# Kernel optimization log

Hardware: AMD Instinct MI355X
Metric: run time of the kernel (lower is better)

Reference implementation:

```python
import jax, jax.numpy as jnp
import numpy as np

N_NODES = 50000
N_EDGES = 800000
D_IN = 96
HID = 128


def _glorot(key, shape):
    fan_in, fan_out = shape[0], shape[1]
    lim = np.sqrt(6.0 / (fan_in + fan_out)).astype(np.float32)
    return jax.random.uniform(key, shape, jnp.float32, -lim, lim)


def setup_inputs() -> dict:
    key = jax.random.key(0)
    ks = jax.random.split(key, 12)
    x = jax.random.normal(ks[0], (N_NODES, D_IN), jnp.float32)
    edge_index = jax.random.randint(ks[1], (2, N_EDGES), 0, N_NODES)
    return {
        "x": x,
        "edge_index": edge_index,
        "W_in": _glorot(ks[2], (D_IN, HID)),
        "b_in": jnp.zeros((HID,), jnp.float32),
        "W1": _glorot(ks[3], (HID, HID)),
        "b1": jnp.zeros((HID,), jnp.float32),
        "W2": _glorot(ks[4], (HID, HID)),
        "b2": jnp.zeros((HID,), jnp.float32),
        "Wm1": _glorot(ks[5], (2 * HID, HID)),
        "bm1": jnp.zeros((HID,), jnp.float32),
        "Wm2": _glorot(ks[6], (HID, 1)),
        "bm2": jnp.zeros((1,), jnp.float32),
    }


def _gcn_conv(h, W, b, src, dst, n_nodes):
    # PyG GCNConv with add_self_loops=True, normalize=True:
    # out = D^{-1/2} (A + I) D^{-1/2} (h W) + b, aggregating x_j (source) into dst.
    loop = jnp.arange(n_nodes)
    row = jnp.concatenate([src, loop])  # source / j
    col = jnp.concatenate([dst, loop])  # target / i
    deg = jax.ops.segment_sum(jnp.ones(row.shape, h.dtype), col, num_segments=n_nodes)
    dinv = jnp.where(deg > 0, jax.lax.rsqrt(deg), 0.0)
    norm = dinv[row] * dinv[col]  # [E+N]
    xw = h @ W  # [N, H]
    msg = xw[row] * norm[:, None]  # gather + scale, [E+N, H]
    out = jax.ops.segment_sum(msg, col, num_segments=n_nodes)  # scatter-add
    return out + b


def reference(x, edge_index, W_in, b_in, W1, b1, W2, b2, Wm1, bm1, Wm2, bm2):
    src, dst = edge_index[0], edge_index[1]
    n = x.shape[0]
    h = jax.nn.relu(x @ W_in + b_in)  # dropout is identity at inference
    h = jax.nn.relu(_gcn_conv(h, W1, b1, src, dst, n))
    h = jax.nn.relu(_gcn_conv(h, W2, b2, src, dst, n))
    ef = jnp.concatenate([h[src], h[dst]], axis=1)  # [E, 2H]
    hid = jax.nn.relu(ef @ Wm1 + bm1)
    logits = (hid @ Wm2 + bm2)[:, 0]  # [E]
    return logits
```

## Files before the change

### kernel.cpp

```cpp
#include <hip/hip_runtime.h>

#define N_NODES 50000
#define N_EDGES 800000
#define D_IN 96
#define HID 128
#define NB 391
#define BCAP 3072

typedef __attribute__((ext_vector_type(8))) _Float16 halfx8;
typedef __attribute__((ext_vector_type(2))) _Float16 half2v;
typedef __attribute__((ext_vector_type(16))) float f32x16;

__global__ __launch_bounds__(256) void bucket_hist_kernel(const int* __restrict__ dst,
                                                          int* __restrict__ bhist) {
    __shared__ int lh[NB];
    int t = threadIdx.x;
    for (int i = t; i < NB; i += 256) lh[i] = 0;
    __syncthreads();
    int base = blockIdx.x * 4096;
#pragma unroll
    for (int i = 0; i < 16; i++) {
        int e = base + i * 256 + t;
        if (e < N_EDGES) atomicAdd(&lh[dst[e] >> 7], 1);
    }
    __syncthreads();
    for (int i = t; i < NB; i += 256) atomicAdd(&bhist[i], lh[i]);
}

__global__ __launch_bounds__(512) void scan_buckets_kernel(const int* __restrict__ bhist,
                                                           int* __restrict__ boff,
                                                           int* __restrict__ bcursor) {
    __shared__ int s[512];
    int t = threadIdx.x;
    int v = (t < NB) ? bhist[t] : 0;
    s[t] = v;
    __syncthreads();
    for (int off = 1; off < 512; off <<= 1) {
        int u = (t >= off) ? s[t - off] : 0;
        __syncthreads();
        s[t] += u;
        __syncthreads();
    }
    if (t < NB) {
        int ex = s[t] - v;
        boff[t] = ex;
        bcursor[t] = ex;
    }
    if (t == NB - 1) boff[NB] = s[t];
}

__global__ __launch_bounds__(512) void bin_kernel(const int* __restrict__ src,
                                                  const int* __restrict__ dst,
                                                  int* __restrict__ bcursor,
                                                  unsigned long long* __restrict__ binned) {
    __shared__ int lh[NB];
    __shared__ int gbs[NB];
    int t = threadIdx.x;
    for (int i = t; i < NB; i += 512) lh[i] = 0;
    __syncthreads();
    int base = blockIdx.x * 8192;
    unsigned long long pk[16];
    int bb[16], rk[16];
#pragma unroll
    for (int i = 0; i < 16; i++) {
        int e = base + i * 512 + t;
        bb[i] = -1;
        if (e < N_EDGES) {
            int s = src[e], d = dst[e];
            int b = d >> 7;
            bb[i] = b;
            pk[i] = ((unsigned long long)s << 27) |
                    ((unsigned long long)(d & 127) << 20) | (unsigned long long)e;
            rk[i] = atomicAdd(&lh[b], 1);
        }
    }
    __syncthreads();
    for (int i = t; i < NB; i += 512) gbs[i] = atomicAdd(&bcursor[i], lh[i]);
    __syncthreads();
#pragma unroll
    for (int i = 0; i < 16; i++) {
        if (bb[i] >= 0) binned[gbs[bb[i]] + rk[i]] = pk[i];
    }
}

__global__ __launch_bounds__(256) void bucket_sort_kernel(const unsigned long long* __restrict__ binned,
                                                          const int* __restrict__ boff,
                                                          int2* __restrict__ ce_se,
                                                          int* __restrict__ ce_dst,
                                                          int* __restrict__ csr_ptr,
                                                          float* __restrict__ dinv) {
    __shared__ unsigned long long ed[BCAP];
    __shared__ int2 sorted[BCAP];
    __shared__ int cntA[128], sc[128];
    int b = blockIdx.x;
    int t = threadIdx.x;
    int base = boff[b];
    int k = boff[b + 1] - base;
    if (k > BCAP) k = BCAP;
    if (t < 128) cntA[t] = 0;
    __syncthreads();
    int rk[12], li[12];
    int nmine = 0;
    for (int i = t; i < k; i += 256) {
        unsigned long long p = binned[base + i];
        ed[i] = p;
        int d = (int)((p >> 20) & 127);
        rk[nmine] = atomicAdd(&cntA[d], 1);
        li[nmine] = i;
        nmine++;
    }
    __syncthreads();
    if (t < 128) sc[t] = cntA[t];
    __syncthreads();
    for (int off = 1; off < 128; off <<= 1) {
        int u = 0;
        if (t < 128 && t >= off) u = sc[t - off];
        __syncthreads();
        if (t < 128) sc[t] += u;
        __syncthreads();
    }
    for (int m = 0; m < nmine; m++) {
        unsigned long long p = ed[li[m]];
        int d = (int)((p >> 20) & 127);
        int pos = sc[d] - cntA[d] + rk[m];
        int srcn = (int)(p >> 27);
        int eid = (int)(p & 0xFFFFF);
        sorted[pos] = make_int2(srcn | (d << 16), eid);
    }
    __syncthreads();
    for (int i = t; i < k; i += 256) {
        int2 se = sorted[i];
        ce_se[base + i] = make_int2(se.x & 0xFFFF, se.y);
        ce_dst[base + i] = (b << 7) + (se.x >> 16);
    }
    if (t < 128) {
        int node = (b << 7) + t;
        if (node < N_NODES) {
            csr_ptr[node] = base + sc[t] - cntA[t];
            dinv[node] = 1.0f / sqrtf((float)(cntA[t] + 1));
        }
    }
    if (b == NB - 1 && t == 0) csr_ptr[N_NODES] = boff[NB];
}

__global__ __launch_bounds__(256) void pack_weights_kernel(const float* __restrict__ W_in,
                                                           const float* __restrict__ W1,
                                                           const float* __restrict__ W2,
                                                           const float* __restrict__ Wm1,
                                                           _Float16* __restrict__ packed) {
    int t = blockIdx.x * 256 + threadIdx.x;
    const float* Wsrc;
    int K, u;
    if (t < 12288)      { Wsrc = W_in;            K = 96;  u = t; }
    else if (t < 28672) { Wsrc = W1;              K = 128; u = t - 12288; }
    else if (t < 45056) { Wsrc = W2;              K = 128; u = t - 28672; }
    else if (t < 61440) { Wsrc = Wm1;             K = 128; u = t - 45056; }
    else                { Wsrc = Wm1 + 128 * 128; K = 128; u = t - 61440; }
    if (t >= 77824) return;
    int steps = K >> 4;
    int cb = u / (steps * 512);
    int rem = u - cb * steps * 512;
    int s = rem >> 9;
    int lane = (rem >> 3) & 63;
    int j = rem & 7;
    int k = s * 16 + ((lane >> 5) << 3) + j;
    int n = (cb << 5) + (lane & 31);
    packed[t] = (_Float16)Wsrc[k * 128 + n];
}

__global__ __launch_bounds__(256) void fused_in_kernel(const float* __restrict__ x,
                                                       const _Float16* __restrict__ WpIn,
                                                       const _Float16* __restrict__ Wp1,
                                                       const float* __restrict__ b_in,
                                                       const float* __restrict__ dinv,
                                                       _Float16* __restrict__ y1, int M) {
    __shared__ _Float16 As[64 * 104];
    __shared__ _Float16 Hs[64 * 136];
    int tid = threadIdx.x;
    int M0 = blockIdx.x * 64;
    for (int i = tid; i < 64 * 24; i += 256) {
        int r = i / 24, c = i - r * 24;
        float4 v = make_float4(0.f, 0.f, 0.f, 0.f);
        int row = M0 + r;
        if (row < M) v = *(const float4*)&x[(size_t)row * 96 + c * 4];
        half2v a = {(_Float16)v.x, (_Float16)v.y};
        half2v b = {(_Float16)v.z, (_Float16)v.w};
        *(half2v*)&As[r * 104 + c * 4] = a;
        *(half2v*)&As[r * 104 + c * 4 + 2] = b;
    }
    __syncthreads();

    int wave = tid >> 6, lane = tid & 63;
    int rb = wave & 1;
    int cb0 = (wave >> 1) * 2;
    int colA = cb0 * 32 + (lane & 31);
    int colB = colA + 32;
    {
        const halfx8* bp0 = (const halfx8*)WpIn + (size_t)cb0 * 6 * 64 + lane;
        const halfx8* bp1 = bp0 + (size_t)6 * 64;
        const _Float16* arow = &As[(rb * 32 + (lane & 31)) * 104 + ((lane >> 5) << 3)];
        f32x16 acc0 = {}, acc1 = {};
#pragma unroll
        for (int s = 0; s < 6; s++) {
            halfx8 a = *(const halfx8*)&arow[s * 16];
            acc0 = __builtin_amdgcn_mfma_f32_32x32x16_f16(a, bp0[s * 64], acc0, 0, 0, 0);
            acc1 = __builtin_amdgcn_mfma_f32_32x32x16_f16(a, bp1[s * 64], acc1, 0, 0, 0);
        }
        float bA = b_in[colA], bB = b_in[colB];
#pragma unroll
        for (int r = 0; r < 16; r++) {
            int rl = (r & 3) + 8 * (r >> 2) + 4 * (lane >> 5);
            int lrow = rb * 32 + rl;
            Hs[lrow * 136 + colA] = (_Float16)fmaxf(acc0[r] + bA, 0.f);
            Hs[lrow * 136 + colB] = (_Float16)fmaxf(acc1[r] + bB, 0.f);
        }
    }
    __syncthreads();
    {
        const halfx8* bp0 = (const halfx8*)Wp1 + (size_t)cb0 * 8 * 64 + lane;
        const halfx8* bp1 = bp0 + (size_t)8 * 64;
        const _Float16* arow = &Hs[(rb * 32 + (lane & 31)) * 136 + ((lane >> 5) << 3)];
        f32x16 acc0 = {}, acc1 = {};
#pragma unroll
        for (int s = 0; s < 8; s++) {
            halfx8 a = *(const halfx8*)&arow[s * 16];
            acc0 = __builtin_amdgcn_mfma_f32_32x32x16_f16(a, bp0[s * 64], acc0, 0, 0, 0);
            acc1 = __builtin_amdgcn_mfma_f32_32x32x16_f16(a, bp1[s * 64], acc1, 0, 0, 0);
        }
#pragma unroll
        for (int r = 0; r < 16; r++) {
            int rl = (r & 3) + 8 * (r >> 2) + 4 * (lane >> 5);
            int grow = M0 + rb * 32 + rl;
            if (grow < M) {
                float sc = dinv[grow];
                y1[(size_t)grow * 128 + colA] = (_Float16)(acc0[r] * sc);
                y1[(size_t)grow * 128 + colB] = (_Float16)(acc1[r] * sc);
            }
        }
    }
}

__global__ __launch_bounds__(256) void gemm_f16_kernel(const _Float16* __restrict__ A,
                                                       const _Float16* __restrict__ Wp,
                                                       const float* __restrict__ bias,
                                                       const float* __restrict__ rowscale,
                                                       _Float16* __restrict__ out,
                                                       int M, int K, int steps, int dorelu) {
    __shared__ _Float16 As[64 * 136];
    int tid = threadIdx.x;
    int M0 = blockIdx.x * 64;
    int stride = K + 8;
    int CH = K >> 3;
    int tot = 64 * CH;
    for (int i = tid; i < tot; i += 256) {
        int r = i / CH, c = i - r * CH;
        uint4 v = make_uint4(0, 0, 0, 0);
        int row = M0 + r;
        if (row < M) v = *(const uint4*)&A[(size_t)row * K + c * 8];
        *(uint4*)&As[r * stride + c * 8] = v;
    }
    __syncthreads();

    int wave = tid >> 6, lane = tid & 63;
    int rb = wave & 1;
    int cb0 = (wave >> 1) * 2;
    const halfx8* bp0 = (const halfx8*)Wp + (size_t)cb0 * steps * 64 + lane;
    const halfx8* bp1 = bp0 + (size_t)steps * 64;
    const _Float16* arow = &As[(rb * 32 + (lane & 31)) * stride + ((lane >> 5) << 3)];
    f32x16 acc0 = {}, acc1 = {};
    for (int s = 0; s < steps; s++) {
        halfx8 a = *(const halfx8*)&arow[s * 16];
        acc0 = __builtin_amdgcn_mfma_f32_32x32x16_f16(a, bp0[s * 64], acc0, 0, 0, 0);
        acc1 = __builtin_amdgcn_mfma_f32_32x32x16_f16(a, bp1[s * 64], acc1, 0, 0, 0);
    }

    int colA = cb0 * 32 + (lane & 31);
    int colB = colA + 32;
    float bA = bias ? bias[colA] : 0.f;
    float bB = bias ? bias[colB] : 0.f;
#pragma unroll
    for (int r = 0; r < 16; r++) {
        int rl = (r & 3) + 8 * (r >> 2) + 4 * (lane >> 5);
        int grow = M0 + rb * 32 + rl;
        if (grow < M) {
            float sc = rowscale ? rowscale[grow] : 1.f;
            float v0 = (acc0[r] + bA) * sc;
            float v1 = (acc1[r] + bB) * sc;
            if (dorelu) { v0 = fmaxf(v0, 0.f); v1 = fmaxf(v1, 0.f); }
            out[(size_t)grow * 128 + colA] = (_Float16)v0;
            out[(size_t)grow * 128 + colB] = (_Float16)v1;
        }
    }
}

__global__ __launch_bounds__(256) void gemm_uv_kernel(const _Float16* __restrict__ A,
                                                      const _Float16* __restrict__ WpU,
                                                      const _Float16* __restrict__ WpV,
                                                      const float* __restrict__ bm1,
                                                      _Float16* __restrict__ U,
                                                      _Float16* __restrict__ V,
                                                      int M) {
    const int K = 128, steps = 8;
    __shared__ _Float16 As[64 * 136];
    int tid = threadIdx.x;
    int M0 = blockIdx.x * 64;
    int stride = K + 8;
    for (int i = tid; i < 64 * 16; i += 256) {
        int r = i >> 4, c = i & 15;
        uint4 v = make_uint4(0, 0, 0, 0);
        int row = M0 + r;
        if (row < M) v = *(const uint4*)&A[(size_t)row * K + c * 8];
        *(uint4*)&As[r * stride + c * 8] = v;
    }
    __syncthreads();

    int wave = tid >> 6, lane = tid & 63;
    int rb = wave & 1;
    int cb0 = (wave >> 1) * 2;
    const halfx8* bu0 = (const halfx8*)WpU + (size_t)cb0 * steps * 64 + lane;
    const halfx8* bu1 = bu0 + (size_t)steps * 64;
    const halfx8* bv0 = (const halfx8*)WpV + (size_t)cb0 * steps * 64 + lane;
    const halfx8* bv1 = bv0 + (size_t)steps * 64;
    const _Float16* arow = &As[(rb * 32 + (lane & 31)) * stride + ((lane >> 5) << 3)];
    f32x16 au0 = {}, au1 = {}, av0 = {}, av1 = {};
    for (int s = 0; s < steps; s++) {
        halfx8 a = *(const halfx8*)&arow[s * 16];
        au0 = __builtin_amdgcn_mfma_f32_32x32x16_f16(a, bu0[s * 64], au0, 0, 0, 0);
        au1 = __builtin_amdgcn_mfma_f32_32x32x16_f16(a, bu1[s * 64], au1, 0, 0, 0);
        av0 = __builtin_amdgcn_mfma_f32_32x32x16_f16(a, bv0[s * 64], av0, 0, 0, 0);
        av1 = __builtin_amdgcn_mfma_f32_32x32x16_f16(a, bv1[s * 64], av1, 0, 0, 0);
    }

    int colA = cb0 * 32 + (lane & 31);
    int colB = colA + 32;
    float bA = bm1[colA], bB = bm1[colB];
#pragma unroll
    for (int r = 0; r < 16; r++) {
        int rl = (r & 3) + 8 * (r >> 2) + 4 * (lane >> 5);
        int grow = M0 + rb * 32 + rl;
        if (grow < M) {
            U[(size_t)grow * 128 + colA] = (_Float16)(au0[r] + bA);
            U[(size_t)grow * 128 + colB] = (_Float16)(au1[r] + bB);
            V[(size_t)grow * 128 + colA] = (_Float16)av0[r];
            V[(size_t)grow * 128 + colB] = (_Float16)av1[r];
        }
    }
}

__global__ __launch_bounds__(256) void aggregate_kernel(const _Float16* __restrict__ y,
                                                        const float* __restrict__ dinv,
                                                        const int* __restrict__ ptr,
                                                        const int2* __restrict__ ce_se,
                                                        const float* __restrict__ bias,
                                                        _Float16* __restrict__ out) {
    int node = blockIdx.x * 4 + (threadIdx.x >> 6);
    int lane = threadIdx.x & 63;
    int c = lane * 2;
    float di = dinv[node];
    half2v self = ((const half2v*)&y[(size_t)node * 128])[lane];
    float a0 = (float)self.x, a1 = (float)self.y;
    float b0 = 0.f, b1 = 0.f, c0 = 0.f, c1 = 0.f, d0 = 0.f, d1 = 0.f;
    int s0 = ptr[node], s1 = ptr[node + 1];
    int j = s0;
    for (; j + 7 < s1; j += 8) {
        int n0 = ce_se[j].x, n1 = ce_se[j + 1].x, n2 = ce_se[j + 2].x, n3 = ce_se[j + 3].x;
        int n4 = ce_se[j + 4].x, n5 = ce_se[j + 5].x, n6 = ce_se[j + 6].x, n7 = ce_se[j + 7].x;
        half2v v0 = ((const half2v*)&y[(size_t)n0 * 128])[lane];
        half2v v1 = ((const half2v*)&y[(size_t)n1 * 128])[lane];
        half2v v2 = ((const half2v*)&y[(size_t)n2 * 128])[lane];
        half2v v3 = ((const half2v*)&y[(size_t)n3 * 128])[lane];
        half2v v4 = ((const half2v*)&y[(size_t)n4 * 128])[lane];
        half2v v5 = ((const half2v*)&y[(size_t)n5 * 128])[lane];
        half2v v6 = ((const half2v*)&y[(size_t)n6 * 128])[lane];
        half2v v7 = ((const half2v*)&y[(size_t)n7 * 128])[lane];
        a0 += (float)v0.x + (float)v4.x; a1 += (float)v0.y + (float)v4.y;
        b0 += (float)v1.x + (float)v5.x; b1 += (float)v1.y + (float)v5.y;
        c0 += (float)v2.x + (float)v6.x; c1 += (float)v2.y + (float)v6.y;
        d0 += (float)v3.x + (float)v7.x; d1 += (float)v3.y + (float)v7.y;
    }
    for (; j < s1; j++) {
        int n = ce_se[j].x;
        half2v v = ((const half2v*)&y[(size_t)n * 128])[lane];
        a0 += (float)v.x; a1 += (float)v.y;
    }
    float2 bv = *(const float2*)&bias[c];
    float o0 = fmaxf(di * (a0 + b0 + c0 + d0) + bv.x, 0.f);
    float o1 = fmaxf(di * (a1 + b1 + c1 + d1) + bv.y, 0.f);
    half2v ov = {(_Float16)o0, (_Float16)o1};
    ((half2v*)&out[(size_t)node * 128])[lane] = ov;
}

__global__ __launch_bounds__(256) void edge_mlp_kernel(const _Float16* __restrict__ Ub,
                                                       const _Float16* __restrict__ Vb,
                                                       const int2* __restrict__ ce_se,
                                                       const int* __restrict__ ce_dst,
                                                       const float* __restrict__ Wm2,
                                                       const float* __restrict__ bm2,
                                                       float* __restrict__ out) {
    __shared__ int ssrc[64], sdst[64], seid[64];
    int tid = threadIdx.x;
    int e0 = blockIdx.x * 64;
    if (tid < 64) {
        int2 se = ce_se[e0 + tid];
        ssrc[tid] = se.x;
        seid[tid] = se.y;
    } else if (tid < 128) {
        sdst[tid - 64] = ce_dst[e0 + tid - 64];
    }
    __syncthreads();
    int g = tid >> 4;
    int l = tid & 15;
    int ga = g, gb = g + 16, gc = g + 32, gd = g + 48;
    halfx8 u0 = *(const halfx8*)&Ub[(size_t)ssrc[ga] * 128 + l * 8];
    halfx8 v0 = *(const halfx8*)&Vb[(size_t)sdst[ga] * 128 + l * 8];
    halfx8 u1 = *(const halfx8*)&Ub[(size_t)ssrc[gb] * 128 + l * 8];
    halfx8 v1 = *(const halfx8*)&Vb[(size_t)sdst[gb] * 128 + l * 8];
    halfx8 u2 = *(const halfx8*)&Ub[(size_t)ssrc[gc] * 128 + l * 8];
    halfx8 v2 = *(const halfx8*)&Vb[(size_t)sdst[gc] * 128 + l * 8];
    halfx8 u3 = *(const halfx8*)&Ub[(size_t)ssrc[gd] * 128 + l * 8];
    halfx8 v3 = *(const halfx8*)&Vb[(size_t)sdst[gd] * 128 + l * 8];
    float4 w0 = *(const float4*)&Wm2[l * 8];
    float4 w1 = *(const float4*)&Wm2[l * 8 + 4];
    float wm[8] = {w0.x, w0.y, w0.z, w0.w, w1.x, w1.y, w1.z, w1.w};
    float p0 = 0.f, p1 = 0.f, p2 = 0.f, p3 = 0.f;
#pragma unroll
    for (int t = 0; t < 8; t++) {
        p0 = fmaf(fmaxf((float)u0[t] + (float)v0[t], 0.f), wm[t], p0);
        p1 = fmaf(fmaxf((float)u1[t] + (float)v1[t], 0.f), wm[t], p1);
        p2 = fmaf(fmaxf((float)u2[t] + (float)v2[t], 0.f), wm[t], p2);
        p3 = fmaf(fmaxf((float)u3[t] + (float)v3[t], 0.f), wm[t], p3);
    }
#pragma unroll
    for (int d = 1; d < 16; d <<= 1) {
        p0 += __shfl_xor(p0, d);
        p1 += __shfl_xor(p1, d);
        p2 += __shfl_xor(p2, d);
        p3 += __shfl_xor(p3, d);
    }
    if (l == 0) {
        float bb = bm2[0];
        out[seid[ga]] = p0 + bb;
        out[seid[gb]] = p1 + bb;
        out[seid[gc]] = p2 + bb;
        out[seid[gd]] = p3 + bb;
    }
}

extern "C" void kernel_launch(void* const* d_in, const int* in_sizes, int n_in,
                              void* d_out, int out_size, void* d_ws, size_t ws_size,
                              hipStream_t stream) {
    const float* x    = (const float*)d_in[0];
    const int* eidx   = (const int*)d_in[1];
    const float* W_in = (const float*)d_in[2];
    const float* b_in = (const float*)d_in[3];
    const float* W1   = (const float*)d_in[4];
    const float* b1   = (const float*)d_in[5];
    const float* W2   = (const float*)d_in[6];
    const float* b2   = (const float*)d_in[7];
    const float* Wm1  = (const float*)d_in[8];
    const float* bm1  = (const float*)d_in[9];
    const float* Wm2  = (const float*)d_in[10];
    const float* bm2  = (const float*)d_in[11];
    float* out = (float*)d_out;
    const int* src = eidx;
    const int* dst = eidx + N_EDGES;

    char* w = (char*)d_ws;
    size_t off = 0;
    auto alloc = [&](size_t bytes) -> char* {
        char* p = w + off;
        off = (off + bytes + 255) & ~(size_t)255;
        return p;
    };
    int* bhist    = (int*)alloc((size_t)NB * 4);
    int* boff     = (int*)alloc((size_t)(NB + 1) * 4);
    int* bcursor  = (int*)alloc((size_t)NB * 4);
    int* csr_ptr  = (int*)alloc((size_t)(N_NODES + 1) * 4);
    float* dinv   = (float*)alloc((size_t)N_NODES * 4);
    unsigned long long* binned = (unsigned long long*)alloc((size_t)N_EDGES * 8);
    int2* ce_se   = (int2*)alloc((size_t)N_EDGES * 8);
    int* ce_dst   = (int*)alloc((size_t)N_EDGES * 4);
    _Float16* Wp  = (_Float16*)alloc((size_t)77824 * 2);
    _Float16* y1  = (_Float16*)alloc((size_t)N_NODES * HID * 2);
    _Float16* y2  = (_Float16*)alloc((size_t)N_NODES * HID * 2);
    _Float16* hbuf = (_Float16*)alloc((size_t)N_NODES * HID * 2);
    _Float16* Ub  = (_Float16*)alloc((size_t)N_NODES * HID * 2);
    _Float16* Vb  = (_Float16*)alloc((size_t)N_NODES * HID * 2);

    const _Float16* WpIn  = Wp;
    const _Float16* Wp1   = Wp + 12288;
    const _Float16* Wp2   = Wp + 28672;
    const _Float16* WpM1a = Wp + 45056;
    const _Float16* WpM1b = Wp + 61440;

    hipMemsetAsync(bhist, 0, (size_t)NB * 4, stream);
    bucket_hist_kernel<<<196, 256, 0, stream>>>(dst, bhist);
    scan_buckets_kernel<<<1, 512, 0, stream>>>(bhist, boff, bcursor);
    bin_kernel<<<98, 512, 0, stream>>>(src, dst, bcursor, binned);
    bucket_sort_kernel<<<NB, 256, 0, stream>>>(binned, boff, ce_se, ce_dst, csr_ptr, dinv);
    pack_weights_kernel<<<(77824 + 255) / 256, 256, 0, stream>>>(W_in, W1, W2, Wm1, Wp);

    int gblocks = (N_NODES + 63) / 64;
    fused_in_kernel<<<gblocks, 256, 0, stream>>>(x, WpIn, Wp1, b_in, dinv, y1, N_NODES);
    aggregate_kernel<<<N_NODES / 4, 256, 0, stream>>>(y1, dinv, csr_ptr, ce_se, b1, hbuf);
    gemm_f16_kernel<<<gblocks, 256, 0, stream>>>(hbuf, Wp2, nullptr, dinv, y2,
                                                 N_NODES, HID, 8, 0);
    aggregate_kernel<<<N_NODES / 4, 256, 0, stream>>>(y2, dinv, csr_ptr, ce_se, b2, hbuf);
    gemm_uv_kernel<<<gblocks, 256, 0, stream>>>(hbuf, WpM1a, WpM1b, bm1, Ub, Vb, N_NODES);
    edge_mlp_kernel<<<N_EDGES / 64, 256, 0, stream>>>(Ub, Vb, ce_se, ce_dst, Wm2, bm2, out);
}
```

Measured before the change: 277.9 us.

## Split edge arrays into SoA, halve GEMM row tiles, use 32-lane aggregation

The packed int2 (src, eid) CSR array is split into separate src and eid arrays, so aggregation only streams the 4-byte source indices and reads half as many index bytes. Aggregation now gives each node 32 lanes that load 4 halves apiece, covering 8 nodes per block, which puts more gather loads in flight and raises node parallelism. The three GEMM kernels shrink their row tile from 64 to 32, with each wave owning one 32-column block. This doubles the block count for better occupancy but reduces weight reuse per block.

```diff
diff --git a/kernel.cpp b/kernel.cpp
--- a/kernel.cpp
+++ b/kernel.cpp
@@ -8,6 +8,7 @@
 #define BCAP 3072
 
 typedef __attribute__((ext_vector_type(8))) _Float16 halfx8;
+typedef __attribute__((ext_vector_type(4))) _Float16 half4v;
 typedef __attribute__((ext_vector_type(2))) _Float16 half2v;
 typedef __attribute__((ext_vector_type(16))) float f32x16;
 
@@ -85,7 +86,8 @@
 
 __global__ __launch_bounds__(256) void bucket_sort_kernel(const unsigned long long* __restrict__ binned,
                                                           const int* __restrict__ boff,
-                                                          int2* __restrict__ ce_se,
+                                                          int* __restrict__ ce_src,
+                                                          int* __restrict__ ce_eid,
                                                           int* __restrict__ ce_dst,
                                                           int* __restrict__ csr_ptr,
                                                           float* __restrict__ dinv) {
@@ -130,7 +132,8 @@
     __syncthreads();
     for (int i = t; i < k; i += 256) {
         int2 se = sorted[i];
-        ce_se[base + i] = make_int2(se.x & 0xFFFF, se.y);
+        ce_src[base + i] = se.x & 0xFFFF;
+        ce_eid[base + i] = se.y;
         ce_dst[base + i] = (b << 7) + (se.x >> 16);
     }
     if (t < 128) {
@@ -174,11 +177,11 @@
                                                        const float* __restrict__ b_in,
                                                        const float* __restrict__ dinv,
                                                        _Float16* __restrict__ y1, int M) {
-    __shared__ _Float16 As[64 * 104];
-    __shared__ _Float16 Hs[64 * 136];
+    __shared__ _Float16 As[32 * 104];
+    __shared__ _Float16 Hs[32 * 136];
     int tid = threadIdx.x;
-    int M0 = blockIdx.x * 64;
-    for (int i = tid; i < 64 * 24; i += 256) {
+    int M0 = blockIdx.x * 32;
+    for (int i = tid; i < 32 * 24; i += 256) {
         int r = i / 24, c = i - r * 24;
         float4 v = make_float4(0.f, 0.f, 0.f, 0.f);
         int row = M0 + r;
@@ -191,50 +194,39 @@
     __syncthreads();
 
     int wave = tid >> 6, lane = tid & 63;
-    int rb = wave & 1;
-    int cb0 = (wave >> 1) * 2;
-    int colA = cb0 * 32 + (lane & 31);
-    int colB = colA + 32;
+    int col = wave * 32 + (lane & 31);
     {
-        const halfx8* bp0 = (const halfx8*)WpIn + (size_t)cb0 * 6 * 64 + lane;
-        const halfx8* bp1 = bp0 + (size_t)6 * 64;
-        const _Float16* arow = &As[(rb * 32 + (lane & 31)) * 104 + ((lane >> 5) << 3)];
-        f32x16 acc0 = {}, acc1 = {};
+        const halfx8* bp = (const halfx8*)WpIn + (size_t)wave * 6 * 64 + lane;
+        const _Float16* arow = &As[(lane & 31) * 104 + ((lane >> 5) << 3)];
+        f32x16 acc = {};
 #pragma unroll
         for (int s = 0; s < 6; s++) {
             halfx8 a = *(const halfx8*)&arow[s * 16];
-            acc0 = __builtin_amdgcn_mfma_f32_32x32x16_f16(a, bp0[s * 64], acc0, 0, 0, 0);
-            acc1 = __builtin_amdgcn_mfma_f32_32x32x16_f16(a, bp1[s * 64], acc1, 0, 0, 0);
-        }
-        float bA = b_in[colA], bB = b_in[colB];
+            acc = __builtin_amdgcn_mfma_f32_32x32x16_f16(a, bp[s * 64], acc, 0, 0, 0);
+        }
+        float bA = b_in[col];
 #pragma unroll
         for (int r = 0; r < 16; r++) {
             int rl = (r & 3) + 8 * (r >> 2) + 4 * (lane >> 5);
-            int lrow = rb * 32 + rl;
-            Hs[lrow * 136 + colA] = (_Float16)fmaxf(acc0[r] + bA, 0.f);
-            Hs[lrow * 136 + colB] = (_Float16)fmaxf(acc1[r] + bB, 0.f);
+            Hs[rl * 136 + col] = (_Float16)fmaxf(acc[r] + bA, 0.f);
         }
     }
     __syncthreads();
     {
-        const halfx8* bp0 = (const halfx8*)Wp1 + (size_t)cb0 * 8 * 64 + lane;
-        const halfx8* bp1 = bp0 + (size_t)8 * 64;
-        const _Float16* arow = &Hs[(rb * 32 + (lane & 31)) * 136 + ((lane >> 5) << 3)];
-        f32x16 acc0 = {}, acc1 = {};
+        const halfx8* bp = (const halfx8*)Wp1 + (size_t)wave * 8 * 64 + lane;
+        const _Float16* arow = &Hs[(lane & 31) * 136 + ((lane >> 5) << 3)];
+        f32x16 acc = {};
 #pragma unroll
         for (int s = 0; s < 8; s++) {
             halfx8 a = *(const halfx8*)&arow[s * 16];
-            acc0 = __builtin_amdgcn_mfma_f32_32x32x16_f16(a, bp0[s * 64], acc0, 0, 0, 0);
-            acc1 = __builtin_amdgcn_mfma_f32_32x32x16_f16(a, bp1[s * 64], acc1, 0, 0, 0);
+            acc = __builtin_amdgcn_mfma_f32_32x32x16_f16(a, bp[s * 64], acc, 0, 0, 0);
         }
 #pragma unroll
         for (int r = 0; r < 16; r++) {
             int rl = (r & 3) + 8 * (r >> 2) + 4 * (lane >> 5);
-            int grow = M0 + rb * 32 + rl;
+            int grow = M0 + rl;
             if (grow < M) {
-                float sc = dinv[grow];
-                y1[(size_t)grow * 128 + colA] = (_Float16)(acc0[r] * sc);
-                y1[(size_t)grow * 128 + colB] = (_Float16)(acc1[r] * sc);
+                y1[(size_t)grow * 128 + col] = (_Float16)(acc[r] * dinv[grow]);
             }
         }
     }
@@ -246,12 +238,12 @@
                                                        const float* __restrict__ rowscale,
                                                        _Float16* __restrict__ out,
                                                        int M, int K, int steps, int dorelu) {
-    __shared__ _Float16 As[64 * 136];
+    __shared__ _Float16 As[32 * 136];
     int tid = threadIdx.x;
-    int M0 = blockIdx.x * 64;
+    int M0 = blockIdx.x * 32;
     int stride = K + 8;
     int CH = K >> 3;
-    int tot = 64 * CH;
+    int tot = 32 * CH;
     for (int i = tid; i < tot; i += 256) {
         int r = i / CH, c = i - r * CH;
         uint4 v = make_uint4(0, 0, 0, 0);
@@ -262,33 +254,24 @@
     __syncthreads();
 
     int wave = tid >> 6, lane = tid & 63;
-    int rb = wave & 1;
-    int cb0 = (wave >> 1) * 2;
-    const halfx8* bp0 = (const halfx8*)Wp + (size_t)cb0 * steps * 64 + lane;
-    const halfx8* bp1 = bp0 + (size_t)steps * 64;
-    const _Float16* arow = &As[(rb * 32 + (lane & 31)) * stride + ((lane >> 5) << 3)];
-    f32x16 acc0 = {}, acc1 = {};
+    const halfx8* bp = (const halfx8*)Wp + (size_t)wave * steps * 64 + lane;
+    const _Float16* arow = &As[(lane & 31) * stride + ((lane >> 5) << 3)];
+    f32x16 acc = {};
     for (int s = 0; s < steps; s++) {
         halfx8 a = *(const halfx8*)&arow[s * 16];
-        acc0 = __builtin_amdgcn_mfma_f32_32x32x16_f16(a, bp0[s * 64], acc0, 0, 0, 0);
-        acc1 = __builtin_amdgcn_mfma_f32_32x32x16_f16(a, bp1[s * 64], acc1, 0, 0, 0);
-    }
-
-    int colA = cb0 * 32 + (lane & 31);
-    int colB = colA + 32;
-    float bA = bias ? bias[colA] : 0.f;
-    float bB = bias ? bias[colB] : 0.f;
+        acc = __builtin_amdgcn_mfma_f32_32x32x16_f16(a, bp[s * 64], acc, 0, 0, 0);
+    }
+    int col = wave * 32 + (lane & 31);
+    float bA = bias ? bias[col] : 0.f;
 #pragma unroll
     for (int r = 0; r < 16; r++) {
         int rl = (r & 3) + 8 * (r >> 2) + 4 * (lane >> 5);
-        int grow = M0 + rb * 32 + rl;
+        int grow = M0 + rl;
         if (grow < M) {
             float sc = rowscale ? rowscale[grow] : 1.f;
-            float v0 = (acc0[r] + bA) * sc;
-            float v1 = (acc1[r] + bB) * sc;
-            if (dorelu) { v0 = fmaxf(v0, 0.f); v1 = fmaxf(v1, 0.f); }
-            out[(size_t)grow * 128 + colA] = (_Float16)v0;
-            out[(size_t)grow * 128 + colB] = (_Float16)v1;
+            float v0 = (acc[r] + bA) * sc;
+            if (dorelu) v0 = fmaxf(v0, 0.f);
+            out[(size_t)grow * 128 + col] = (_Float16)v0;
         }
     }
 }
@@ -301,11 +284,11 @@
                                                       _Float16* __restrict__ V,
                                                       int M) {
     const int K = 128, steps = 8;
-    __shared__ _Float16 As[64 * 136];
+    __shared__ _Float16 As[32 * 136];
     int tid = threadIdx.x;
-    int M0 = blockIdx.x * 64;
+    int M0 = blockIdx.x * 32;
     int stride = K + 8;
-    for (int i = tid; i < 64 * 16; i += 256) {
+    for (int i = tid; i < 32 * 16; i += 256) {
         int r = i >> 4, c = i & 15;
         uint4 v = make_uint4(0, 0, 0, 0);
         int row = M0 + r;
@@ -315,34 +298,25 @@
     __syncthreads();
 
     int wave = tid >> 6, lane = tid & 63;
-    int rb = wave & 1;
-    int cb0 = (wave >> 1) * 2;
-    const halfx8* bu0 = (const halfx8*)WpU + (size_t)cb0 * steps * 64 + lane;
-    const halfx8* bu1 = bu0 + (size_t)steps * 64;
-    const halfx8* bv0 = (const halfx8*)WpV + (size_t)cb0 * steps * 64 + lane;
-    const halfx8* bv1 = bv0 + (size_t)steps * 64;
-    const _Float16* arow = &As[(rb * 32 + (lane & 31)) * stride + ((lane >> 5) << 3)];
-    f32x16 au0 = {}, au1 = {}, av0 = {}, av1 = {};
+    const halfx8* bu = (const halfx8*)WpU + (size_t)wave * steps * 64 + lane;
+    const halfx8* bv = (const halfx8*)WpV + (size_t)wave * steps * 64 + lane;
+    const _Float16* arow = &As[(lane & 31) * stride + ((lane >> 5) << 3)];
+    f32x16 au = {}, av = {};
+#pragma unroll
     for (int s = 0; s < steps; s++) {
         halfx8 a = *(const halfx8*)&arow[s * 16];
-        au0 = __builtin_amdgcn_mfma_f32_32x32x16_f16(a, bu0[s * 64], au0, 0, 0, 0);
-        au1 = __builtin_amdgcn_mfma_f32_32x32x16_f16(a, bu1[s * 64], au1, 0, 0, 0);
-        av0 = __builtin_amdgcn_mfma_f32_32x32x16_f16(a, bv0[s * 64], av0, 0, 0, 0);
-        av1 = __builtin_amdgcn_mfma_f32_32x32x16_f16(a, bv1[s * 64], av1, 0, 0, 0);
-    }
-
-    int colA = cb0 * 32 + (lane & 31);
-    int colB = colA + 32;
-    float bA = bm1[colA], bB = bm1[colB];
+        au = __builtin_amdgcn_mfma_f32_32x32x16_f16(a, bu[s * 64], au, 0, 0, 0);
+        av = __builtin_amdgcn_mfma_f32_32x32x16_f16(a, bv[s * 64], av, 0, 0, 0);
+    }
+    int col = wave * 32 + (lane & 31);
+    float bA = bm1[col];
 #pragma unroll
     for (int r = 0; r < 16; r++) {
         int rl = (r & 3) + 8 * (r >> 2) + 4 * (lane >> 5);
-        int grow = M0 + rb * 32 + rl;
+        int grow = M0 + rl;
         if (grow < M) {
-            U[(size_t)grow * 128 + colA] = (_Float16)(au0[r] + bA);
-            U[(size_t)grow * 128 + colB] = (_Float16)(au1[r] + bB);
-            V[(size_t)grow * 128 + colA] = (_Float16)av0[r];
-            V[(size_t)grow * 128 + colB] = (_Float16)av1[r];
+            U[(size_t)grow * 128 + col] = (_Float16)(au[r] + bA);
+            V[(size_t)grow * 128 + col] = (_Float16)av[r];
         }
     }
 }
@@ -350,49 +324,55 @@
 __global__ __launch_bounds__(256) void aggregate_kernel(const _Float16* __restrict__ y,
                                                         const float* __restrict__ dinv,
                                                         const int* __restrict__ ptr,
-                                                        const int2* __restrict__ ce_se,
+                                                        const int* __restrict__ ce_src,
                                                         const float* __restrict__ bias,
                                                         _Float16* __restrict__ out) {
-    int node = blockIdx.x * 4 + (threadIdx.x >> 6);
-    int lane = threadIdx.x & 63;
-    int c = lane * 2;
+    int node = blockIdx.x * 8 + (threadIdx.x >> 5);
+    int l = threadIdx.x & 31;
     float di = dinv[node];
-    half2v self = ((const half2v*)&y[(size_t)node * 128])[lane];
-    float a0 = (float)self.x, a1 = (float)self.y;
-    float b0 = 0.f, b1 = 0.f, c0 = 0.f, c1 = 0.f, d0 = 0.f, d1 = 0.f;
+    half4v self = ((const half4v*)&y[(size_t)node * 128])[l];
+    float a0 = (float)self[0], a1 = (float)self[1], a2 = (float)self[2], a3 = (float)self[3];
+    float b0 = 0.f, b1 = 0.f, b2 = 0.f, b3 = 0.f;
     int s0 = ptr[node], s1 = ptr[node + 1];
     int j = s0;
     for (; j + 7 < s1; j += 8) {
-        int n0 = ce_se[j].x, n1 = ce_se[j + 1].x, n2 = ce_se[j + 2].x, n3 = ce_se[j + 3].x;
-        int n4 = ce_se[j + 4].x, n5 = ce_se[j + 5].x, n6 = ce_se[j + 6].x, n7 = ce_se[j + 7].x;
-        half2v v0 = ((const half2v*)&y[(size_t)n0 * 128])[lane];
-        half2v v1 = ((const half2v*)&y[(size_t)n1 * 128])[lane];
-        half2v v2 = ((const half2v*)&y[(size_t)n2 * 128])[lane];
-        half2v v3 = ((const half2v*)&y[(size_t)n3 * 128])[lane];
-        half2v v4 = ((const half2v*)&y[(size_t)n4 * 128])[lane];
-        half2v v5 = ((const half2v*)&y[(size_t)n5 * 128])[lane];
-        half2v v6 = ((const half2v*)&y[(size_t)n6 * 128])[lane];
-        half2v v7 = ((const half2v*)&y[(size_t)n7 * 128])[lane];
-        a0 += (float)v0.x + (float)v4.x; a1 += (float)v0.y + (float)v4.y;
-        b0 += (float)v1.x + (float)v5.x; b1 += (float)v1.y + (float)v5.y;
-        c0 += (float)v2.x + (float)v6.x; c1 += (float)v2.y + (float)v6.y;
-        d0 += (float)v3.x + (float)v7.x; d1 += (float)v3.y + (float)v7.y;
+        int n0 = ce_src[j], n1 = ce_src[j + 1], n2 = ce_src[j + 2], n3 = ce_src[j + 3];
+        int n4 = ce_src[j + 4], n5 = ce_src[j + 5], n6 = ce_src[j + 6], n7 = ce_src[j + 7];
+        half4v v0 = ((const half4v*)&y[(size_t)n0 * 128])[l];
+        half4v v1 = ((const half4v*)&y[(size_t)n1 * 128])[l];
+        half4v v2 = ((const half4v*)&y[(size_t)n2 * 128])[l];
+        half4v v3 = ((const half4v*)&y[(size_t)n3 * 128])[l];
+        half4v v4 = ((const half4v*)&y[(size_t)n4 * 128])[l];
+        half4v v5 = ((const half4v*)&y[(size_t)n5 * 128])[l];
+        half4v v6 = ((const half4v*)&y[(size_t)n6 * 128])[l];
+        half4v v7 = ((const half4v*)&y[(size_t)n7 * 128])[l];
+        a0 += (float)v0[0] + (float)v2[0] + (float)v4[0] + (float)v6[0];
+        a1 += (float)v0[1] + (float)v2[1] + (float)v4[1] + (float)v6[1];
+        a2 += (float)v0[2] + (float)v2[2] + (float)v4[2] + (float)v6[2];
+        a3 += (float)v0[3] + (float)v2[3] + (float)v4[3] + (float)v6[3];
+        b0 += (float)v1[0] + (float)v3[0] + (float)v5[0] + (float)v7[0];
+        b1 += (float)v1[1] + (float)v3[1] + (float)v5[1] + (float)v7[1];
+        b2 += (float)v1[2] + (float)v3[2] + (float)v5[2] + (float)v7[2];
+        b3 += (float)v1[3] + (float)v3[3] + (float)v5[3] + (float)v7[3];
     }
     for (; j < s1; j++) {
-        int n = ce_se[j].x;
-        half2v v = ((const half2v*)&y[(size_t)n * 128])[lane];
-        a0 += (float)v.x; a1 += (float)v.y;
-    }
-    float2 bv = *(const float2*)&bias[c];
-    float o0 = fmaxf(di * (a0 + b0 + c0 + d0) + bv.x, 0.f);
-    float o1 = fmaxf(di * (a1 + b1 + c1 + d1) + bv.y, 0.f);
-    half2v ov = {(_Float16)o0, (_Float16)o1};
-    ((half2v*)&out[(size_t)node * 128])[lane] = ov;
+        int n = ce_src[j];
+        half4v v = ((const half4v*)&y[(size_t)n * 128])[l];
+        a0 += (float)v[0]; a1 += (float)v[1]; a2 += (float)v[2]; a3 += (float)v[3];
+    }
+    float4 bv = *(const float4*)&bias[l * 4];
+    half4v ov;
+    ov[0] = (_Float16)fmaxf(di * (a0 + b0) + bv.x, 0.f);
+    ov[1] = (_Float16)fmaxf(di * (a1 + b1) + bv.y, 0.f);
+    ov[2] = (_Float16)fmaxf(di * (a2 + b2) + bv.z, 0.f);
+    ov[3] = (_Float16)fmaxf(di * (a3 + b3) + bv.w, 0.f);
+    ((half4v*)&out[(size_t)node * 128])[l] = ov;
 }
 
 __global__ __launch_bounds__(256) void edge_mlp_kernel(const _Float16* __restrict__ Ub,
                                                        const _Float16* __restrict__ Vb,
-                                                       const int2* __restrict__ ce_se,
+                                                       const int* __restrict__ ce_src,
+                                                       const int* __restrict__ ce_eid,
                                                        const int* __restrict__ ce_dst,
                                                        const float* __restrict__ Wm2,
                                                        const float* __restrict__ bm2,
@@ -401,9 +381,8 @@
     int tid = threadIdx.x;
     int e0 = blockIdx.x * 64;
     if (tid < 64) {
-        int2 se = ce_se[e0 + tid];
-        ssrc[tid] = se.x;
-        seid[tid] = se.y;
+        ssrc[tid] = ce_src[e0 + tid];
+        seid[tid] = ce_eid[e0 + tid];
     } else if (tid < 128) {
         sdst[tid - 64] = ce_dst[e0 + tid - 64];
     }
@@ -478,7 +457,8 @@
     int* csr_ptr  = (int*)alloc((size_t)(N_NODES + 1) * 4);
     float* dinv   = (float*)alloc((size_t)N_NODES * 4);
     unsigned long long* binned = (unsigned long long*)alloc((size_t)N_EDGES * 8);
-    int2* ce_se   = (int2*)alloc((size_t)N_EDGES * 8);
+    int* ce_src   = (int*)alloc((size_t)N_EDGES * 4);
+    int* ce_eid   = (int*)alloc((size_t)N_EDGES * 4);
     int* ce_dst   = (int*)alloc((size_t)N_EDGES * 4);
     _Float16* Wp  = (_Float16*)alloc((size_t)77824 * 2);
     _Float16* y1  = (_Float16*)alloc((size_t)N_NODES * HID * 2);
@@ -497,15 +477,17 @@
     bucket_hist_kernel<<<196, 256, 0, stream>>>(dst, bhist);
     scan_buckets_kernel<<<1, 512, 0, stream>>>(bhist, boff, bcursor);
     bin_kernel<<<98, 512, 0, stream>>>(src, dst, bcursor, binned);
-    bucket_sort_kernel<<<NB, 256, 0, stream>>>(binned, boff, ce_se, ce_dst, csr_ptr, dinv);
+    bucket_sort_kernel<<<NB, 256, 0, stream>>>(binned, boff, ce_src, ce_eid, ce_dst,
+                                               csr_ptr, dinv);
     pack_weights_kernel<<<(77824 + 255) / 256, 256, 0, stream>>>(W_in, W1, W2, Wm1, Wp);
 
-    int gblocks = (N_NODES + 63) / 64;
+    int gblocks = (N_NODES + 31) / 32;
     fused_in_kernel<<<gblocks, 256, 0, stream>>>(x, WpIn, Wp1, b_in, dinv, y1, N_NODES);
-    aggregate_kernel<<<N_NODES / 4, 256, 0, stream>>>(y1, dinv, csr_ptr, ce_se, b1, hbuf);
+    aggregate_kernel<<<N_NODES / 8, 256, 0, stream>>>(y1, dinv, csr_ptr, ce_src, b1, hbuf);
     gemm_f16_kernel<<<gblocks, 256, 0, stream>>>(hbuf, Wp2, nullptr, dinv, y2,
                                                  N_NODES, HID, 8, 0);
-    aggregate_kernel<<<N_NODES / 4, 256, 0, stream>>>(y2, dinv, csr_ptr, ce_se, b2, hbuf);
+    aggregate_kernel<<<N_NODES / 8, 256, 0, stream>>>(y2, dinv, csr_ptr, ce_src, b2, hbuf);
     gemm_uv_kernel<<<gblocks, 256, 0, stream>>>(hbuf, WpM1a, WpM1b, bm1, Ub, Vb, N_NODES);
-    edge_mlp_kernel<<<N_EDGES / 64, 256, 0, stream>>>(Ub, Vb, ce_se, ce_dst, Wm2, bm2, out);
-}
+    edge_mlp_kernel<<<N_EDGES / 64, 256, 0, stream>>>(Ub, Vb, ce_src, ce_eid, ce_dst,
+                                                      Wm2, bm2, out);
+}
```

Measured after the change: 260.3 us. 6.3% less time.
